# Kernel optimization log

Measured on AMD Instinct MI355X. Metric: run time of the kernel, lower is better.

## Reference

```python
import jax, jax.numpy as jnp
import numpy as np

B, S, H = 2, 2048, 2048
NH, NKV, HD = 16, 4, 128
SCALING = HD ** -0.5


def rotate_half(x):
    x1, x2 = jnp.split(x, 2, axis=-1)
    return jnp.concatenate((-x2, x1), axis=-1)


def apply_rope(t, cos, sin):
    # t: [B, nh, S, HD]; cos/sin: [B, S, HD] -> unsqueeze head dim
    c = cos[:, None, :, :]
    s = sin[:, None, :, :]
    return t * c + rotate_half(t) * s


def setup_inputs() -> dict:
    key = jax.random.key(0)
    k1, k2, k3, k4, k5 = jax.random.split(key, 5)
    hidden_states = jax.random.normal(k1, (B, S, H), dtype=jnp.float32)
    # real RoPE tables
    inv_freq = 1.0 / (10000.0 ** (jnp.arange(0, HD, 2, dtype=jnp.float32) / HD))
    pos = jnp.arange(S, dtype=jnp.float32)
    freqs = jnp.einsum('s,d->sd', pos, inv_freq)              # [S, HD/2]
    emb = jnp.concatenate((freqs, freqs), axis=-1)            # [S, HD]
    cos = jnp.broadcast_to(jnp.cos(emb)[None], (B, S, HD))
    sin = jnp.broadcast_to(jnp.sin(emb)[None], (B, S, HD))
    # additive causal mask [B, 1, S, S]
    causal = jnp.triu(jnp.full((S, S), -1e9, dtype=jnp.float32), k=1)
    attention_mask = jnp.broadcast_to(causal[None, None], (B, 1, S, S))
    sc = 0.02
    wq = jax.random.normal(k2, (NH * HD, H), dtype=jnp.float32) * sc
    wk = jax.random.normal(k3, (NKV * HD, H), dtype=jnp.float32) * sc
    wv = jax.random.normal(k4, (NKV * HD, H), dtype=jnp.float32) * sc
    wo = jax.random.normal(k5, (H, NH * HD), dtype=jnp.float32) * sc
    return {"hidden_states": hidden_states, "cos": cos, "sin": sin,
            "attention_mask": attention_mask, "wq": wq, "wk": wk, "wv": wv, "wo": wo}


def reference(hidden_states, cos, sin, attention_mask, wq, wk, wv, wo):
    x = hidden_states
    # fused-style QKV projections (nn.Linear: x @ W.T), split heads -> [B, nh, S, HD]
    q = (x @ wq.T).reshape(B, S, NH, HD).transpose(0, 2, 1, 3)
    k = (x @ wk.T).reshape(B, S, NKV, HD).transpose(0, 2, 1, 3)
    v = (x @ wv.T).reshape(B, S, NKV, HD).transpose(0, 2, 1, 3)
    q = apply_rope(q, cos, sin)
    k = apply_rope(k, cos, sin)
    # GQA: repeat KV heads (repeat_kv)
    n_rep = NH // NKV
    k = jnp.repeat(k, n_rep, axis=1)
    v = jnp.repeat(v, n_rep, axis=1)
    scores = jnp.einsum('bhqd,bhkd->bhqk', q, k) * SCALING + attention_mask
    attn = jax.nn.softmax(scores.astype(jnp.float32), axis=-1).astype(q.dtype)
    out = jnp.einsum('bhqk,bhkd->bhqd', attn, v)
    out = out.transpose(0, 2, 1, 3).reshape(B, S, NH * HD)
    out = out @ wo.T
    return (out, attn)
```

## Files before the change

### kernel.cpp

```cpp
#include <hip/hip_runtime.h>
#include <cstdint>
#include <cstddef>

typedef __bf16 bf16;
typedef __attribute__((ext_vector_type(8))) __bf16 bf16x8;
typedef __attribute__((ext_vector_type(4))) __bf16 bf16x4;
typedef __attribute__((ext_vector_type(4))) float f32x4;

constexpr int B_ = 2, S_ = 2048, H_ = 2048, NH_ = 16, NKV_ = 4, HD_ = 128;
constexpr float SCALE_ = 0.08838834764831845f;

#define GLDS16(g, l)                                                        \
  __builtin_amdgcn_global_load_lds(                                         \
      (const __attribute__((address_space(1))) void*)(g),                   \
      (__attribute__((address_space(3))) void*)(l), 16, 0, 0)

#define VMCNT0 asm volatile("s_waitcnt vmcnt(0)" ::: "memory")
#define VMCNT8 asm volatile("s_waitcnt vmcnt(8)" ::: "memory")
#define SCHED0 __builtin_amdgcn_sched_barrier(0)
#define BAR __builtin_amdgcn_s_barrier()

__device__ inline void nt_store4(float* p, f32x4 v) {
  __builtin_nontemporal_store(v, (f32x4*)p);
}

__global__ void cvt_all(const float* __restrict__ hs, const float* __restrict__ wq,
                        const float* __restrict__ wk, const float* __restrict__ wv,
                        const float* __restrict__ wo, bf16* __restrict__ xb,
                        bf16* __restrict__ w3b, bf16* __restrict__ wob) {
  const int stride = gridDim.x * blockDim.x;
  for (int i = blockIdx.x * blockDim.x + threadIdx.x; i < 4718592; i += stride) {
    const float4* s; bf16x4* d; int j;
    if (i < 2097152)      { s = (const float4*)hs; d = (bf16x4*)xb;            j = i; }
    else if (i < 3145728) { s = (const float4*)wq; d = (bf16x4*)w3b;           j = i - 2097152; }
    else if (i < 3407872) { s = (const float4*)wk; d = (bf16x4*)w3b + 1048576; j = i - 3145728; }
    else if (i < 3670016) { s = (const float4*)wv; d = (bf16x4*)w3b + 1310720; j = i - 3407872; }
    else                  { s = (const float4*)wo; d = (bf16x4*)wob;           j = i - 3670016; }
    float4 v = s[j];
    bf16x4 o;
    o[0] = (bf16)v.x; o[1] = (bf16)v.y; o[2] = (bf16)v.z; o[3] = (bf16)v.w;
    d[j] = o;
  }
}

template <int EPI>
__global__ __launch_bounds__(256) void gemm_bt(const bf16* __restrict__ A,
                                               const bf16* __restrict__ Bm, int K,
                                               bf16* __restrict__ qb, bf16* __restrict__ kb,
                                               bf16* __restrict__ vtb, float* __restrict__ Cout) {
  __shared__ __align__(16) bf16 As[128 * 64];
  __shared__ __align__(16) bf16 Bs[128 * 64];
  const int tid = threadIdx.x;
  const int lane = tid & 63;
  const int wid = tid >> 6;
  const int fid = blockIdx.y * 32 + blockIdx.x;
  const int nwg = gridDim.y * 32;
  const int swz = (fid & 7) * (nwg >> 3) + (fid >> 3);
  const int m0 = (swz & 31) * 128;
  const int n0 = (swz >> 5) * 128;
  const int wm = (wid >> 1) * 64, wn = (wid & 1) * 64;
  const int r = lane & 15, g = lane >> 4;
  f32x4 acc[4][4] = {};

#pragma unroll 1
  for (int kt = 0; kt < K; kt += 64) {
    __syncthreads();
#pragma unroll
    for (int i = 0; i < 4; ++i) {
      int cb = wid * 256 + i * 64;
      int c64 = cb + lane;
      int row = c64 >> 3, cs = (c64 & 7) ^ (row & 7);
      GLDS16(A + (size_t)(m0 + row) * K + kt + cs * 8, As + cb * 8);
      GLDS16(Bm + (size_t)(n0 + row) * K + kt + cs * 8, Bs + cb * 8);
    }
    VMCNT0;
    __syncthreads();
#pragma unroll
    for (int ks = 0; ks < 2; ++ks) {
      bf16x8 af[4], bfr[4];
#pragma unroll
      for (int fm = 0; fm < 4; ++fm)
        af[fm] = *(const bf16x8*)(As + (wm + fm * 16 + r) * 64 + (((ks * 4 + g) ^ (r & 7)) << 3));
#pragma unroll
      for (int fn = 0; fn < 4; ++fn)
        bfr[fn] = *(const bf16x8*)(Bs + (wn + fn * 16 + r) * 64 + (((ks * 4 + g) ^ (r & 7)) << 3));
#pragma unroll
      for (int fm = 0; fm < 4; ++fm)
#pragma unroll
        for (int fn = 0; fn < 4; ++fn)
          acc[fm][fn] = __builtin_amdgcn_mfma_f32_16x16x32_bf16(af[fm], bfr[fn], acc[fm][fn], 0, 0, 0);
    }
  }

#pragma unroll
  for (int fm = 0; fm < 4; ++fm)
#pragma unroll
    for (int fn = 0; fn < 4; ++fn)
#pragma unroll
      for (int rr = 0; rr < 4; ++rr) {
        int mm = m0 + wm + fm * 16 + g * 4 + rr;
        int nn = n0 + wn + fn * 16 + r;
        float v = acc[fm][fn][rr];
        if (EPI == 1) {
          Cout[(size_t)mm * 2048 + nn] = v;
        } else {
          int b = mm >> 11, s = mm & (S_ - 1);
          int d = nn & 127;
          if (nn < 2048) {
            int hh = nn >> 7;
            qb[(((size_t)b * NH_ + hh) * S_ + s) * HD_ + d] = (bf16)v;
          } else if (nn < 2560) {
            int hh = (nn - 2048) >> 7;
            kb[(((size_t)b * NKV_ + hh) * S_ + s) * HD_ + d] = (bf16)v;
          } else {
            int hh = (nn - 2560) >> 7;
            vtb[(((size_t)b * NKV_ + hh) * HD_ + d) * S_ + s] = (bf16)v;
          }
        }
      }
}

__global__ void rope_k_kernel(bf16* __restrict__ kb, const float* __restrict__ cosp,
                              const float* __restrict__ sinp) {
  const int NK = B_ * NKV_ * S_;
  int t = blockIdx.x * blockDim.x + threadIdx.x;
  if (t >= NK * 8) return;
  const int oct = t & 7, rid = t >> 3;
  bf16* base = kb + (size_t)rid * HD_;
  const int s = rid & (S_ - 1);
  const int b = rid >> 13;
  const int d = oct * 8;
  const float* cp = cosp + ((size_t)b * S_ + s) * HD_ + d;
  const float* sp = sinp + ((size_t)b * S_ + s) * HD_ + d;
  float4 c0 = *(const float4*)cp, c1 = *(const float4*)(cp + 4);
  float4 s0 = *(const float4*)sp, s1 = *(const float4*)(sp + 4);
  float cc[8] = {c0.x, c0.y, c0.z, c0.w, c1.x, c1.y, c1.z, c1.w};
  float ss[8] = {s0.x, s0.y, s0.z, s0.w, s1.x, s1.y, s1.z, s1.w};
  bf16x8 x1 = *(const bf16x8*)(base + d);
  bf16x8 x2 = *(const bf16x8*)(base + d + 64);
  bf16x8 o1, o2;
#pragma unroll
  for (int i = 0; i < 8; ++i) {
    float a = (float)x1[i], bb = (float)x2[i];
    o1[i] = (bf16)(a * cc[i] - bb * ss[i]);
    o2[i] = (bf16)(bb * cc[i] + a * ss[i]);
  }
  *(bf16x8*)(base + d) = o1;
  *(bf16x8*)(base + d + 64) = o2;
}

__global__ __launch_bounds__(256, 2) void attn_kernel(const bf16* __restrict__ qb,
                                                      const bf16* __restrict__ kb,
                                                      const bf16* __restrict__ vtb,
                                                      const float* __restrict__ cosp,
                                                      const float* __restrict__ sinp,
                                                      bf16* __restrict__ aob,
                                                      float* __restrict__ attn_out) {
  __shared__ __align__(16) bf16 Ks[2][64 * 128];
  __shared__ __align__(16) bf16 Vs[2][128 * 64];
  __shared__ __align__(16) bf16 Ps[64 * 64];
  const int x7 = blockIdx.x & 7;
  const int k = blockIdx.x >> 3;
  const int qt = (k < 32) ? (31 - k) : (k - 32);
  const int g2 = x7 + ((k >> 5) << 3);
  const int b = g2 >> 3;
  const int kh = (g2 >> 1) & 3;
  const int hp = g2 & 1;
  const int h0 = kh * 4 + hp * 2;
  const int q0 = qt * 64;
  const int nt = qt + 1;
  const int tid = threadIdx.x, lane = tid & 63, wid = tid >> 6;
  const int r = lane & 15, g = lane >> 4;

  const bf16* kbase = kb + ((size_t)b * NKV_ + kh) * S_ * HD_;
  const bf16* vbase = vtb + ((size_t)b * NKV_ + kh) * (size_t)HD_ * S_;
  size_t arow0[2];
#pragma unroll
  for (int hh = 0; hh < 2; ++hh)
    arow0[hh] = ((size_t)(b * NH_ + h0 + hh) * S_ + q0) * S_;

  auto stageK = [&](int kt, int cc) {
#pragma unroll
    for (int i = 0; i < 4; ++i) {
      int base = i * 256 + wid * 64;
      int idx = base + lane;
      int row = idx >> 4, ch = (idx & 15) ^ (row & 7);
      GLDS16(kbase + (size_t)(kt * 64 + row) * HD_ + ch * 8, &Ks[cc][base * 8]);
    }
  };
  auto stageV = [&](int kt, int cc) {
#pragma unroll
    for (int i = 0; i < 4; ++i) {
      int base = i * 256 + wid * 64;
      int idx = base + lane;
      int row = idx >> 3, ch = (idx & 7) ^ (row & 7);
      GLDS16(vbase + (size_t)row * S_ + kt * 64 + ch * 8, &Vs[cc][base * 8]);
    }
  };

  bf16x8 qreg[2][4];
  {
    const int srow = q0 + wid * 16 + r;
    const float* cp = cosp + ((size_t)b * S_ + srow) * HD_;
    const float* sp = sinp + ((size_t)b * S_ + srow) * HD_;
    float cc[2][8], ss[2][8];
#pragma unroll
    for (int hf = 0; hf < 2; ++hf) {
      const int d0 = hf * 32 + g * 8;
      float4 ca = *(const float4*)(cp + d0), cb2 = *(const float4*)(cp + d0 + 4);
      float4 sa = *(const float4*)(sp + d0), sb2 = *(const float4*)(sp + d0 + 4);
      cc[hf][0] = ca.x; cc[hf][1] = ca.y; cc[hf][2] = ca.z; cc[hf][3] = ca.w;
      cc[hf][4] = cb2.x; cc[hf][5] = cb2.y; cc[hf][6] = cb2.z; cc[hf][7] = cb2.w;
      ss[hf][0] = sa.x; ss[hf][1] = sa.y; ss[hf][2] = sa.z; ss[hf][3] = sa.w;
      ss[hf][4] = sb2.x; ss[hf][5] = sb2.y; ss[hf][6] = sb2.z; ss[hf][7] = sb2.w;
    }
#pragma unroll
    for (int hh = 0; hh < 2; ++hh) {
      const bf16* qsrc = qb + ((size_t)(b * NH_ + h0 + hh) * S_ + q0) * HD_;
#pragma unroll
      for (int ks = 0; ks < 4; ++ks)
        qreg[hh][ks] = *(const bf16x8*)(qsrc + (wid * 16 + r) * HD_ + ks * 32 + g * 8);
#pragma unroll
      for (int hf = 0; hf < 2; ++hf) {
        bf16x8 lo = qreg[hh][hf], hi = qreg[hh][hf + 2];
#pragma unroll
        for (int i = 0; i < 8; ++i) {
          float a = (float)lo[i], bb = (float)hi[i];
          qreg[hh][hf][i] = (bf16)(a * cc[hf][i] - bb * ss[hf][i]);
          qreg[hh][hf + 2][i] = (bf16)(bb * cc[hf][i] + a * ss[hf][i]);
        }
      }
    }
  }

  float lsum[2] = {0.f, 0.f};
  stageK(0, 0);
  VMCNT0; BAR;
  int c = 0;
#pragma unroll 1
  for (int kt = 0; kt < nt; ++kt) {
    const bool hn = (kt + 1 < nt);
    if (hn) { stageK(kt + 1, c ^ 1); SCHED0; }
#pragma unroll
    for (int hh = 0; hh < 2; ++hh) {
      f32x4 sacc[4] = {};
      __builtin_amdgcn_s_setprio(1);
#pragma unroll
      for (int ks = 0; ks < 4; ++ks)
#pragma unroll
        for (int fn = 0; fn < 4; ++fn) {
          bf16x8 kk = *(const bf16x8*)(&Ks[c][(fn * 16 + r) * 128 + (((ks * 4 + g) ^ (r & 7)) << 3)]);
          sacc[fn] = __builtin_amdgcn_mfma_f32_16x16x32_bf16(kk, qreg[hh][ks], sacc[fn], 0, 0, 0);
        }
      __builtin_amdgcn_s_setprio(0);
      float ts = 0.f;
      if (kt == nt - 1) {
#pragma unroll
        for (int fn = 0; fn < 4; ++fn)
#pragma unroll
          for (int rr = 0; rr < 4; ++rr) {
            bool msk = (fn * 16 + g * 4 + rr) > (wid * 16 + r);
            ts += msk ? 0.f : __expf(sacc[fn][rr] * SCALE_);
          }
      } else {
#pragma unroll
        for (int fn = 0; fn < 4; ++fn)
#pragma unroll
          for (int rr = 0; rr < 4; ++rr) ts += __expf(sacc[fn][rr] * SCALE_);
      }
      ts += __shfl_xor(ts, 16);
      ts += __shfl_xor(ts, 32);
      lsum[hh] += ts;
    }
    if (hn) { VMCNT0; }
    BAR;
    c ^= 1;
  }
  float rl[2] = {1.0f / lsum[0], 1.0f / lsum[1]};

  f32x4 oacc[2][8] = {};
  stageK(0, 0);
  stageV(0, 0);
  VMCNT0; BAR;
  c = 0;
#pragma unroll 1
  for (int kt = 0; kt < nt; ++kt) {
    const int k0 = kt * 64;
    const bool hn = (kt + 1 < nt);
    if (hn) { stageK(kt + 1, c ^ 1); stageV(kt + 1, c ^ 1); SCHED0; }
    const bool last = (kt == nt - 1);
#pragma unroll
    for (int hh = 0; hh < 2; ++hh) {
      f32x4 sacc[4] = {};
      __builtin_amdgcn_s_setprio(1);
#pragma unroll
      for (int ks = 0; ks < 4; ++ks)
#pragma unroll
        for (int fn = 0; fn < 4; ++fn) {
          bf16x8 kk = *(const bf16x8*)(&Ks[c][(fn * 16 + r) * 128 + (((ks * 4 + g) ^ (r & 7)) << 3)]);
          sacc[fn] = __builtin_amdgcn_mfma_f32_16x16x32_bf16(kk, qreg[hh][ks], sacc[fn], 0, 0, 0);
        }
      __builtin_amdgcn_s_setprio(0);
      const int prow = (wid * 16 + r) * 64;
#pragma unroll
      for (int fn = 0; fn < 4; ++fn) {
        f32x4 pv4;
        bf16x4 pk;
#pragma unroll
        for (int rr = 0; rr < 4; ++rr) {
          bool msk = last && ((fn * 16 + g * 4 + rr) > (wid * 16 + r));
          float f = msk ? 0.f : __expf(sacc[fn][rr] * SCALE_) * rl[hh];
          pv4[rr] = f;
          pk[rr] = (bf16)f;
        }
        nt_store4(attn_out + arow0[hh] + (size_t)(wid * 16 + r) * S_ + k0 + fn * 16 + g * 4, pv4);
        *(bf16x4*)(&Ps[prow + ((((fn << 1) | (g >> 1)) ^ (r & 7)) << 3) + ((g & 1) << 2)]) = pk;
      }
      __builtin_amdgcn_s_setprio(1);
#pragma unroll
      for (int ks = 0; ks < 2; ++ks) {
        bf16x8 pa = *(const bf16x8*)(&Ps[prow + (((ks * 4 + g) ^ (r & 7)) << 3)]);
#pragma unroll
        for (int fn = 0; fn < 8; ++fn) {
          bf16x8 vv = *(const bf16x8*)(&Vs[c][(fn * 16 + r) * 64 + (((ks * 4 + g) ^ (r & 7)) << 3)]);
          oacc[hh][fn] = __builtin_amdgcn_mfma_f32_16x16x32_bf16(pa, vv, oacc[hh][fn], 0, 0, 0);
        }
      }
      __builtin_amdgcn_s_setprio(0);
    }
    if (hn) { VMCNT8; }
    BAR;
    c ^= 1;
  }

#pragma unroll
  for (int hh = 0; hh < 2; ++hh)
#pragma unroll
    for (int fn = 0; fn < 8; ++fn)
#pragma unroll
      for (int rr = 0; rr < 4; ++rr) {
        int q = q0 + wid * 16 + g * 4 + rr;
        aob[((size_t)b * S_ + q) * 2048 + (h0 + hh) * HD_ + fn * 16 + r] = (bf16)oacc[hh][fn][rr];
      }

  const int nzero = 62 - 2 * qt;
#pragma unroll 1
  for (int z = 0; z < nzero; ++z) {
    int hh = (z >= 31 - qt) ? 1 : 0;
    int ktz = qt + 1 + (hh ? z - (31 - qt) : z);
    float* zdst = attn_out + arow0[hh] + ktz * 64;
    f32x4 zv = {0.f, 0.f, 0.f, 0.f};
#pragma unroll
    for (int i = 0; i < 4; ++i) {
      int idx = i * 256 + tid;
      nt_store4(zdst + (size_t)(idx >> 4) * S_ + (idx & 15) * 4, zv);
    }
  }
}

extern "C" void kernel_launch(void* const* d_in, const int* in_sizes, int n_in,
                              void* d_out, int out_size, void* d_ws, size_t ws_size,
                              hipStream_t stream) {
  const float* hidden = (const float*)d_in[0];
  const float* cosp = (const float*)d_in[1];
  const float* sinp = (const float*)d_in[2];
  const float* wq = (const float*)d_in[4];
  const float* wk = (const float*)d_in[5];
  const float* wv = (const float*)d_in[6];
  const float* wo = (const float*)d_in[7];
  float* out = (float*)d_out;
  float* attn = out + (size_t)B_ * S_ * H_;

  char* ws = (char*)d_ws;
  bf16* xb  = (bf16*)(ws);
  bf16* w3b = (bf16*)(ws + (16ull << 20));
  bf16* wob = (bf16*)(ws + (28ull << 20));
  bf16* qb  = (bf16*)(ws + (36ull << 20));
  bf16* kb  = (bf16*)(ws + (52ull << 20));
  bf16* vtb = (bf16*)(ws + (56ull << 20));
  bf16* aob = (bf16*)(ws + (60ull << 20));

  cvt_all<<<2048, 256, 0, stream>>>(hidden, wq, wk, wv, wo, xb, w3b, wob);
  gemm_bt<0><<<dim3(32, 24), 256, 0, stream>>>(xb, w3b, 2048, qb, kb, vtb, nullptr);
  rope_k_kernel<<<512, 256, 0, stream>>>(kb, cosp, sinp);
  attn_kernel<<<512, 256, 0, stream>>>(qb, kb, vtb, cosp, sinp, aob, attn);
  gemm_bt<1><<<dim3(32, 16), 256, 0, stream>>>(aob, wob, 2048, nullptr, nullptr, nullptr, out);
}
```

Measured before the change: 340.5 us.

## Replace GEMM with 256x256-tile, 8-wave, double-buffered pipelined kernel

Rewrites the projection GEMMs to use 256x256 output tiles per 512-thread block with double-buffered LDS. Global-to-LDS loads for upcoming k-tiles are interleaved across eight compute phases using partial vmcnt waits and raised wave priority around the MFMA blocks. This aims to hide memory latency and raise reuse per loaded byte. The trade-off is far fewer blocks (192 and 128), which may leave many CUs idle, plus higher register pressure from the 8x4 accumulator tile.

```diff
diff --git a/kernel.cpp b/kernel.cpp
--- a/kernel.cpp
+++ b/kernel.cpp
@@ -16,7 +16,9 @@
       (__attribute__((address_space(3))) void*)(l), 16, 0, 0)
 
 #define VMCNT0 asm volatile("s_waitcnt vmcnt(0)" ::: "memory")
+#define VMCNT6 asm volatile("s_waitcnt vmcnt(6)" ::: "memory")
 #define VMCNT8 asm volatile("s_waitcnt vmcnt(8)" ::: "memory")
+#define LGKM0 asm volatile("s_waitcnt lgkmcnt(0)" ::: "memory")
 #define SCHED0 __builtin_amdgcn_sched_barrier(0)
 #define BAR __builtin_amdgcn_s_barrier()
 
@@ -44,63 +46,110 @@
 }
 
 template <int EPI>
-__global__ __launch_bounds__(256) void gemm_bt(const bf16* __restrict__ A,
-                                               const bf16* __restrict__ Bm, int K,
-                                               bf16* __restrict__ qb, bf16* __restrict__ kb,
-                                               bf16* __restrict__ vtb, float* __restrict__ Cout) {
-  __shared__ __align__(16) bf16 As[128 * 64];
-  __shared__ __align__(16) bf16 Bs[128 * 64];
+__global__ __launch_bounds__(512, 2) void gemm8p(const bf16* __restrict__ Ag,
+                                                 const bf16* __restrict__ Bg, int K,
+                                                 bf16* __restrict__ qb, bf16* __restrict__ kb,
+                                                 bf16* __restrict__ vtb, float* __restrict__ Cout) {
+  __shared__ __align__(16) bf16 As[2][256 * 64];
+  __shared__ __align__(16) bf16 Bs[2][256 * 64];
   const int tid = threadIdx.x;
   const int lane = tid & 63;
   const int wid = tid >> 6;
-  const int fid = blockIdx.y * 32 + blockIdx.x;
-  const int nwg = gridDim.y * 32;
+  const int wr = wid >> 2, wc = wid & 3;
+  const int r = lane & 15, g = lane >> 4;
+  const int fid = blockIdx.x;
+  const int nwg = gridDim.x;
   const int swz = (fid & 7) * (nwg >> 3) + (fid >> 3);
-  const int m0 = (swz & 31) * 128;
-  const int n0 = (swz >> 5) * 128;
-  const int wm = (wid >> 1) * 64, wn = (wid & 1) * 64;
-  const int r = lane & 15, g = lane >> 4;
-  f32x4 acc[4][4] = {};
-
+  const int m0 = (swz & 15) << 8;
+  const int n0 = (swz >> 4) << 8;
+
+  const int NT = K >> 6;
+  const int NITER = NT >> 1;
+
+  const int rowin = wid * 8 + (lane >> 3);
+  const int cs8 = ((lane & 7) ^ ((lane >> 3) & 7)) << 3;
+
+  auto stageA = [&](int kt, int mq, int c) {
+#pragma unroll
+    for (int r2 = 0; r2 < 2; ++r2)
+      GLDS16(Ag + (size_t)(m0 + r2 * 128 + mq * 64 + rowin) * K + kt * 64 + cs8,
+             &As[c][(mq * 128 + r2 * 64 + wid * 8) * 64]);
+  };
+  auto stageB = [&](int kt, int nq, int c) {
+#pragma unroll
+    for (int r2 = 0; r2 < 2; ++r2) {
+      int halfoff = r2 * 64 + rowin;
+      int n = ((halfoff >> 5) << 6) + nq * 32 + (halfoff & 31);
+      GLDS16(Bg + (size_t)(n0 + n) * K + kt * 64 + cs8,
+             &Bs[c][(nq * 128 + r2 * 64 + wid * 8) * 64]);
+    }
+  };
+
+  f32x4 acc[8][4] = {};
+
+  stageB(0, 0, 0); stageA(0, 0, 0); stageA(0, 1, 0);
+  stageB(0, 1, 0); stageB(1, 0, 1); stageA(1, 0, 1);
+  VMCNT6; BAR;
+
+  bf16x8 bfr[2][2];
 #pragma unroll 1
-  for (int kt = 0; kt < K; kt += 64) {
-    __syncthreads();
-#pragma unroll
-    for (int i = 0; i < 4; ++i) {
-      int cb = wid * 256 + i * 64;
-      int c64 = cb + lane;
-      int row = c64 >> 3, cs = (c64 & 7) ^ (row & 7);
-      GLDS16(A + (size_t)(m0 + row) * K + kt + cs * 8, As + cb * 8);
-      GLDS16(Bm + (size_t)(n0 + row) * K + kt + cs * 8, Bs + cb * 8);
-    }
-    VMCNT0;
-    __syncthreads();
-#pragma unroll
-    for (int ks = 0; ks < 2; ++ks) {
-      bf16x8 af[4], bfr[4];
+  for (int t = 0; t < NITER; ++t) {
+    const int t2 = 2 * t;
+    const bool lastI = (t == NITER - 1);
+#pragma unroll
+    for (int ph = 0; ph < 8; ++ph) {
+      if (lastI) { VMCNT0; } else { VMCNT6; }
+      const int tl = ph >> 2;
+      const int p2 = ph & 3;
+      const int mq = p2 & 1, nq = p2 >> 1;
+      bf16x8 af[4][2];
 #pragma unroll
       for (int fm = 0; fm < 4; ++fm)
-        af[fm] = *(const bf16x8*)(As + (wm + fm * 16 + r) * 64 + (((ks * 4 + g) ^ (r & 7)) << 3));
-#pragma unroll
-      for (int fn = 0; fn < 4; ++fn)
-        bfr[fn] = *(const bf16x8*)(Bs + (wn + fn * 16 + r) * 64 + (((ks * 4 + g) ^ (r & 7)) << 3));
+#pragma unroll
+        for (int ks = 0; ks < 2; ++ks)
+          af[fm][ks] = *(const bf16x8*)(
+              &As[tl][(mq * 128 + wr * 64 + fm * 16 + r) * 64 + (((ks * 4 + g) ^ (r & 7)) << 3)]);
+      if (mq == 0) {
+#pragma unroll
+        for (int fn2 = 0; fn2 < 2; ++fn2)
+#pragma unroll
+          for (int ks = 0; ks < 2; ++ks)
+            bfr[fn2][ks] = *(const bf16x8*)(
+                &Bs[tl][(nq * 128 + wc * 32 + fn2 * 16 + r) * 64 + (((ks * 4 + g) ^ (r & 7)) << 3)]);
+      }
+      if (ph == 0)      { stageA(t2 + 1, 1, 1); }
+      else if (ph == 1) { stageB(t2 + 1, 1, 1); }
+      else if (ph == 2) { if (t2 + 2 < NT) stageB(t2 + 2, 0, 0); }
+      else if (ph == 3) { if (t2 + 2 < NT) stageA(t2 + 2, 0, 0); }
+      else if (ph == 4) { if (t2 + 2 < NT) stageA(t2 + 2, 1, 0); }
+      else if (ph == 5) { if (t2 + 2 < NT) stageB(t2 + 2, 1, 0); }
+      else if (ph == 6) { if (t2 + 3 < NT) stageB(t2 + 3, 0, 1); }
+      else              { if (t2 + 3 < NT) stageA(t2 + 3, 0, 1); }
+      BAR;
+      LGKM0; SCHED0;
+      __builtin_amdgcn_s_setprio(1);
 #pragma unroll
       for (int fm = 0; fm < 4; ++fm)
 #pragma unroll
-        for (int fn = 0; fn < 4; ++fn)
-          acc[fm][fn] = __builtin_amdgcn_mfma_f32_16x16x32_bf16(af[fm], bfr[fn], acc[fm][fn], 0, 0, 0);
-    }
-  }
-
-#pragma unroll
-  for (int fm = 0; fm < 4; ++fm)
-#pragma unroll
-    for (int fn = 0; fn < 4; ++fn)
+        for (int fn2 = 0; fn2 < 2; ++fn2)
+#pragma unroll
+          for (int ks = 0; ks < 2; ++ks)
+            acc[mq * 4 + fm][nq * 2 + fn2] = __builtin_amdgcn_mfma_f32_16x16x32_bf16(
+                af[fm][ks], bfr[fn2][ks], acc[mq * 4 + fm][nq * 2 + fn2], 0, 0, 0);
+      __builtin_amdgcn_s_setprio(0);
+      BAR;
+    }
+  }
+
+#pragma unroll
+  for (int fmt = 0; fmt < 8; ++fmt)
+#pragma unroll
+    for (int fnt = 0; fnt < 4; ++fnt)
 #pragma unroll
       for (int rr = 0; rr < 4; ++rr) {
-        int mm = m0 + wm + fm * 16 + g * 4 + rr;
-        int nn = n0 + wn + fn * 16 + r;
-        float v = acc[fm][fn][rr];
+        int mm = m0 + wr * 128 + fmt * 16 + g * 4 + rr;
+        int nn = n0 + wc * 64 + fnt * 16 + r;
+        float v = acc[fmt][fnt][rr];
         if (EPI == 1) {
           Cout[(size_t)mm * 2048 + nn] = v;
         } else {
@@ -381,8 +430,8 @@
   bf16* aob = (bf16*)(ws + (60ull << 20));
 
   cvt_all<<<2048, 256, 0, stream>>>(hidden, wq, wk, wv, wo, xb, w3b, wob);
-  gemm_bt<0><<<dim3(32, 24), 256, 0, stream>>>(xb, w3b, 2048, qb, kb, vtb, nullptr);
+  gemm8p<0><<<192, 512, 0, stream>>>(xb, w3b, 2048, qb, kb, vtb, nullptr);
   rope_k_kernel<<<512, 256, 0, stream>>>(kb, cosp, sinp);
   attn_kernel<<<512, 256, 0, stream>>>(qb, kb, vtb, cosp, sinp, aob, attn);
-  gemm_bt<1><<<dim3(32, 16), 256, 0, stream>>>(aob, wob, 2048, nullptr, nullptr, nullptr, out);
-}
+  gemm8p<1><<<128, 512, 0, stream>>>(aob, wob, 2048, nullptr, nullptr, nullptr, out);
+}
```

Measured after the change: 384.2 us. +12.8%, slower.
